# Performance work log

Hardware: AMD Instinct MI355X
Metric: run time of the kernel (lower is better)

The kernel has to match this reference:

```python
import jax, jax.numpy as jnp
import numpy as np

N_INP = 512
N_HID = 512
BATCH = 64
STEPS = 512


def setup_inputs() -> dict:
    key = jax.random.key(0)
    ks = jax.random.split(key, 7)

    def xavier(k, n_in, n_out):
        bound = np.sqrt(3.0) * np.sqrt(2.0 / float(n_in + n_out))
        return jax.random.uniform(k, (n_in, n_out), jnp.float32, -bound, bound)

    return {
        "inputs": jax.random.normal(ks[0], (BATCH, STEPS, N_INP), jnp.float32),
        "W_xz": xavier(ks[1], N_INP, N_HID),
        "W_hz": xavier(ks[2], N_HID, N_HID),
        "b_z": jnp.zeros((N_HID,), jnp.float32),
        "W_xr": xavier(ks[3], N_INP, N_HID),
        "W_hr": xavier(ks[4], N_HID, N_HID),
        "b_r": jnp.zeros((N_HID,), jnp.float32),
        "W_xh": xavier(ks[5], N_INP, N_HID),
        "W_hh": xavier(ks[6], N_HID, N_HID),
        "b_h": jnp.zeros((N_HID,), jnp.float32),
        "train": 0,
    }


def reference(inputs, W_xz, W_hz, b_z, W_xr, W_hr, b_r, W_xh, W_hh, b_h, train):
    # inputs: (B, T, n_inp). GRU with eval-mode (dropout_rate=0), so the
    # dropout branch in the original forward is a no-op.
    B = inputs.shape[0]
    H0 = jnp.zeros((B, W_hz.shape[0]), inputs.dtype)

    def step(H_t, X_t):
        Z_t = jax.nn.sigmoid(X_t @ W_xz + H_t @ W_hz + b_z)
        R_t = jax.nn.sigmoid(X_t @ W_xr + H_t @ W_hr + b_r)
        H_tilde = jnp.tanh(X_t @ W_xh + (R_t * H_t) @ W_hh + b_h)
        H_new = Z_t * H_t + (1.0 - Z_t) * H_tilde
        return H_new, H_new

    xs = jnp.swapaxes(inputs, 0, 1)  # (T, B, n_inp)
    H_final, outs = jax.lax.scan(step, H0, xs)
    outputs = jnp.swapaxes(outs, 0, 1)  # (B, T, n_hid)
    return outputs, H_final
```

## Files before the change

### kernel.cpp

```cpp
#include <hip/hip_runtime.h>

#define B_   64
#define T_   512
#define KIN  512
#define NH   512
#define KEFF 3072
#define NBLK 64
#define NTHR 512

typedef __attribute__((ext_vector_type(8))) short short8;
typedef __attribute__((ext_vector_type(4))) float f32x4;
typedef __attribute__((ext_vector_type(4))) unsigned int u32x4;

__device__ __forceinline__ unsigned short f2b(float f) {
    union { float f; unsigned int u; } v; v.f = f;
    unsigned int u = v.u;
    return (unsigned short)((u + 0x7FFFu + ((u >> 16) & 1u)) >> 16);
}
__device__ __forceinline__ float b2f(unsigned short h) {
    union { float f; unsigned int u; } v; v.u = ((unsigned int)h) << 16;
    return v.f;
}

__global__ void prepack(const float* __restrict__ Wxz, const float* __restrict__ Whz,
                        const float* __restrict__ Wxr, const float* __restrict__ Whr,
                        const float* __restrict__ Wxh, const float* __restrict__ Whh,
                        unsigned short* __restrict__ Bzr, unsigned short* __restrict__ Bh) {
    int keff = blockIdx.x * 256 + threadIdx.x;
    int n    = blockIdx.y;
    int seg  = keff >> 9;
    int k    = keff & 511;
    const float* src;
    int c;
    if (n < 512)       { c = n;        src = (seg < 3) ? Whz : Wxz; }
    else if (n < 1024) { c = n - 512;  src = (seg < 3) ? Whr : Wxr; }
    else               { c = n - 1024; src = (seg < 3) ? Whh : Wxh; }
    float w = src[k * NH + c];
    unsigned short hi = f2b(w);
    unsigned short o  = (seg == 2 || seg == 5) ? f2b(w - b2f(hi)) : hi;
    if (n < 1024) Bzr[(size_t)n * KEFF + keff] = o;
    else          Bh[(size_t)(n - 1024) * KEFF + keff] = o;
}

__device__ __forceinline__ unsigned int ald32(const unsigned int* p) {
    return __hip_atomic_load(p, __ATOMIC_RELAXED, __HIP_MEMORY_SCOPE_AGENT);
}
__device__ __forceinline__ unsigned long long ald64(const void* p) {
    return __hip_atomic_load((const unsigned long long*)p, __ATOMIC_RELAXED,
                             __HIP_MEMORY_SCOPE_AGENT);
}
__device__ __forceinline__ void ast32(unsigned int* p, unsigned int v) {
    __hip_atomic_store(p, v, __ATOMIC_RELAXED, __HIP_MEMORY_SCOPE_AGENT);
}
__device__ __forceinline__ void ast64(void* p, unsigned long long v) {
    __hip_atomic_store((unsigned long long*)p, v, __ATOMIC_RELAXED,
                       __HIP_MEMORY_SCOPE_AGENT);
}

__device__ __forceinline__ void flag_wait16(const unsigned int* flg,
                                            unsigned int tgt, int fidx) {
    while (1) {
        unsigned int v = ald32(flg + fidx);
        if (__all((int)(v >= tgt))) break;
    }
    __builtin_amdgcn_sched_barrier(0);
}

__device__ __forceinline__ int hp_idx(int m, int c) {
    return m * 512 + (c ^ ((m & 7) << 2));
}

__device__ __forceinline__ void cvt_x8(const float* xr, int kp, short8* ahi, short8* alo) {
    f32x4 x0 = *(const f32x4*)(xr + kp);
    f32x4 x1 = *(const f32x4*)(xr + kp + 4);
#pragma unroll
    for (int i = 0; i < 4; ++i) {
        unsigned short h0 = f2b(x0[i]);
        (*ahi)[i] = (short)h0; (*alo)[i] = (short)f2b(x0[i] - b2f(h0));
        unsigned short h1 = f2b(x1[i]);
        (*ahi)[4 + i] = (short)h1; (*alo)[4 + i] = (short)f2b(x1[i] - b2f(h1));
    }
}

__device__ __forceinline__ void unpackw(u32x4 w0, u32x4 w1, short8* ahi, short8* alo) {
    union { unsigned int u[4]; short8 v; } H, L;
    H.u[0] = __builtin_amdgcn_perm(w0[1], w0[0], 0x05040100u);
    H.u[1] = __builtin_amdgcn_perm(w0[3], w0[2], 0x05040100u);
    H.u[2] = __builtin_amdgcn_perm(w1[1], w1[0], 0x05040100u);
    H.u[3] = __builtin_amdgcn_perm(w1[3], w1[2], 0x05040100u);
    L.u[0] = __builtin_amdgcn_perm(w0[1], w0[0], 0x07060302u);
    L.u[1] = __builtin_amdgcn_perm(w0[3], w0[2], 0x07060302u);
    L.u[2] = __builtin_amdgcn_perm(w1[1], w1[0], 0x07060302u);
    L.u[3] = __builtin_amdgcn_perm(w1[3], w1[2], 0x07060302u);
    *ahi = H.v; *alo = L.v;
}

#define MFMA(a, b, c) __builtin_amdgcn_mfma_f32_16x16x32_bf16((a), (b), (c), 0, 0, 0)

__global__ void __launch_bounds__(NTHR, 2) gru_seq(
    const float* __restrict__ X, const float* __restrict__ bz,
    const float* __restrict__ br, const float* __restrict__ bh,
    float* __restrict__ out, float* __restrict__ Zt,
    unsigned int* __restrict__ HP, unsigned int* __restrict__ RHP,
    const unsigned short* __restrict__ Bzr, const unsigned short* __restrict__ Bh,
    unsigned int* flags) {
    const int bid  = blockIdx.x;
    const int s    = bid & 15;
    const int g    = bid >> 4;
    const int tid  = threadIdx.x;
    const int wv   = tid >> 6;
    const int w4   = wv & 3;
    const bool xc  = wv >= 4;
    const int lane = tid & 63;
    const int fm   = lane & 15;
    const int fkc  = lane >> 4;
    const int fk   = fkc * 8;

    __shared__ unsigned int hbufH[16 * 512];
    __shared__ unsigned int hbufR[16 * 512];
    __shared__ float xp1[2][4][16][16];
    __shared__ float xp2a[2][2][16][16];
    __shared__ float xp2b[2][2][16][16];
    __shared__ float comb[2][256];

    const int c1 = s * 64 + w4 * 16 + fm;
    const unsigned short* Bp1 = Bzr + (size_t)c1 * KEFF;
    const bool isz = (c1 < 512);
    const float bias1 = isz ? bz[c1] : br[c1 - 512];

    const int ti = w4 >> 1, jh = w4 & 1;
    const int c2 = s * 32 + ti * 16 + fm;
    const unsigned short* Bp2 = Bh + (size_t)c2 * KEFF;
    const float bias2 = bh[c2];

    const int key = (fm & 7) << 4;
    const int sw0 = (32 * fkc) ^ key;
    const int sw1 = (32 * fkc + 16) ^ key;

    unsigned int* HPg  = HP  + g * 8192;
    unsigned int* RHPg = RHP + g * 8192;
    float*        Ztg  = Zt  + g * 8192;
    unsigned int* flg  = flags + g * 32;
    const int fidx = (lane < 16) ? lane : 15;

    const float* Xg = X + (size_t)(16 * g + fm) * (T_ * KIN);

    auto xg1 = [&](int tt, int buf) {
        f32x4 acc = {0.f, 0.f, 0.f, 0.f};
        const float* xr = Xg + (size_t)tt * KIN;
#pragma unroll 4
        for (int j = 0; j < 16; ++j) {
            int kp = j * 32 + fk;
            short8 xhi, xlo; cvt_x8(xr, kp, &xhi, &xlo);
            short8 b3 = *(const short8*)(Bp1 + 1536 + kp);
            short8 b4 = *(const short8*)(Bp1 + 2048 + kp);
            short8 b5 = *(const short8*)(Bp1 + 2560 + kp);
            acc = MFMA(xhi, b3, acc); acc = MFMA(xlo, b4, acc); acc = MFMA(xhi, b5, acc);
        }
#pragma unroll
        for (int jj = 0; jj < 4; ++jj) xp1[buf][w4][fkc * 4 + jj][fm] = acc[jj];
    };
    auto xg2 = [&](int tt, int buf) {
        f32x4 acc = {0.f, 0.f, 0.f, 0.f};
        const float* xr = Xg + (size_t)tt * KIN;
#pragma unroll
        for (int j = jh * 8; j < jh * 8 + 8; ++j) {
            int kp = j * 32 + fk;
            short8 xhi, xlo; cvt_x8(xr, kp, &xhi, &xlo);
            short8 b3 = *(const short8*)(Bp2 + 1536 + kp);
            short8 b4 = *(const short8*)(Bp2 + 2048 + kp);
            short8 b5 = *(const short8*)(Bp2 + 2560 + kp);
            acc = MFMA(xhi, b3, acc); acc = MFMA(xlo, b4, acc); acc = MFMA(xhi, b5, acc);
        }
        float (*dst)[16][16] = jh ? xp2b[buf] : xp2a[buf];
#pragma unroll
        for (int jj = 0; jj < 4; ++jj) dst[ti][fkc * 4 + jj][fm] = acc[jj];
    };

    if (xc) { xg1(0, 0); xg2(0, 0); }
    __syncthreads();

    for (int t = 0; t < T_; ++t) {
        const int bufc = t & 1, bufn = bufc ^ 1;
        const unsigned int ep = (unsigned int)t * 2u;
        if (wv == 0 && t) flag_wait16(flg, ep, fidx);
        __syncthreads();
        if (!xc) {
            const char* srcb = (const char*)HPg;
            char* dstb = (char*)hbufH;
#pragma unroll
            for (int i = 0; i < 8; ++i) {
                int r = w4 * 8 + i;
                __builtin_amdgcn_global_load_lds(
                    (const unsigned int*)(srcb + r * 1024 + lane * 16),
                    (unsigned int*)(dstb + r * 1024), 16, 0, 0x11);
            }
            asm volatile("s_waitcnt vmcnt(0)" ::: "memory");
            __builtin_amdgcn_sched_barrier(0);
        }
        __syncthreads();
        if (!xc) {
            f32x4 acc = {0.f, 0.f, 0.f, 0.f};
            const char* sl = (const char*)hbufH + fm * 2048;
#pragma unroll 4
            for (int j = 0; j < 16; ++j) {
                u32x4 w0 = *(const u32x4*)(sl + 128 * j + sw0);
                u32x4 w1 = *(const u32x4*)(sl + 128 * j + sw1);
                short8 ahi, alo; unpackw(w0, w1, &ahi, &alo);
                int kp = j * 32 + fk;
                short8 b0 = *(const short8*)(Bp1 + kp);
                short8 b1 = *(const short8*)(Bp1 + 512 + kp);
                short8 b2 = *(const short8*)(Bp1 + 1024 + kp);
                acc = MFMA(ahi, b0, acc); acc = MFMA(alo, b1, acc); acc = MFMA(ahi, b2, acc);
            }
            if (isz) {
                float gz[4];
#pragma unroll
                for (int jj = 0; jj < 4; ++jj)
                    gz[jj] = 1.f / (1.f + __expf(-(acc[jj] +
                               xp1[bufc][w4][fkc * 4 + jj][fm] + bias1)));
                union { float f[2]; unsigned long long q; } p0, p1;
                p0.f[0] = gz[0]; p0.f[1] = gz[1];
                p1.f[0] = gz[2]; p1.f[1] = gz[3];
                float* zp = Ztg + c1 * 16 + fkc * 4;
                ast64(zp, p0.q); ast64(zp + 2, p1.q);
            } else {
                int cr = c1 - 512;
#pragma unroll
                for (int jj = 0; jj < 4; ++jj) {
                    int mr = fkc * 4 + jj;
                    unsigned int hw = *(const unsigned int*)((const char*)hbufH +
                        mr * 2048 + ((4 * cr) ^ ((mr & 7) << 4)));
                    float h  = b2f((unsigned short)(hw & 0xffffu)) +
                               b2f((unsigned short)(hw >> 16));
                    float gr = 1.f / (1.f + __expf(-(acc[jj] +
                                 xp1[bufc][w4][mr][fm] + bias1)));
                    float rh = gr * h;
                    unsigned short hi = f2b(rh);
                    unsigned short lo = f2b(rh - b2f(hi));
                    ast32(RHPg + hp_idx(mr, cr),
                          (unsigned int)hi | ((unsigned int)lo << 16));
                }
            }
        } else if (t + 1 < T_) {
            xg1(t + 1, bufn);
        }
        __syncthreads();
        if (tid == 0) ast32(flg + s, ep + 1u);
        if (wv == 0) flag_wait16(flg, ep + 1u, fidx);
        else if (xc && t + 1 < T_) xg2(t + 1, bufn);
        __syncthreads();
        unsigned long long zq0 = 0, zq1 = 0;
        if (!xc) {
            if (jh == 0) {
                const float* zp = Ztg + c2 * 16 + fkc * 4;
                zq0 = ald64(zp); zq1 = ald64(zp + 2);
            }
            const char* srcb = (const char*)RHPg;
            char* dstb = (char*)hbufR;
#pragma unroll
            for (int i = 0; i < 8; ++i) {
                int r = w4 * 8 + i;
                __builtin_amdgcn_global_load_lds(
                    (const unsigned int*)(srcb + r * 1024 + lane * 16),
                    (unsigned int*)(dstb + r * 1024), 16, 0, 0x11);
            }
            asm volatile("s_waitcnt vmcnt(0)" ::: "memory");
            __builtin_amdgcn_sched_barrier(0);
        }
        __syncthreads();
        f32x4 acc2 = {0.f, 0.f, 0.f, 0.f};
        if (!xc) {
            const char* sl2 = (const char*)hbufR + fm * 2048;
#pragma unroll
            for (int j = jh * 8; j < jh * 8 + 8; ++j) {
                u32x4 w0 = *(const u32x4*)(sl2 + 128 * j + sw0);
                u32x4 w1 = *(const u32x4*)(sl2 + 128 * j + sw1);
                short8 ahi, alo; unpackw(w0, w1, &ahi, &alo);
                int kp = j * 32 + fk;
                short8 b0 = *(const short8*)(Bp2 + kp);
                short8 b1 = *(const short8*)(Bp2 + 512 + kp);
                short8 b2 = *(const short8*)(Bp2 + 1024 + kp);
                acc2 = MFMA(ahi, b0, acc2); acc2 = MFMA(alo, b1, acc2); acc2 = MFMA(ahi, b2, acc2);
            }
            if (jh == 1) {
#pragma unroll
                for (int jj = 0; jj < 4; ++jj)
                    comb[ti][(fkc * 4 + jj) * 16 + fm] = acc2[jj];
            }
        }
        __syncthreads();
        if (!xc && jh == 0) {
            union { unsigned long long q; float f[2]; } z0, z1;
            z0.q = zq0; z1.q = zq1;
            float zv[4] = {z0.f[0], z0.f[1], z1.f[0], z1.f[1]};
#pragma unroll
            for (int jj = 0; jj < 4; ++jj) {
                int mr = fkc * 4 + jj;
                unsigned int hw = *(const unsigned int*)((const char*)hbufH +
                    mr * 2048 + ((4 * c2) ^ ((mr & 7) << 4)));
                float h   = b2f((unsigned short)(hw & 0xffffu)) +
                            b2f((unsigned short)(hw >> 16));
                float pre = acc2[jj] + comb[ti][mr * 16 + fm] +
                            xp2a[bufc][ti][mr][fm] + xp2b[bufc][ti][mr][fm] + bias2;
                float e   = __expf(-2.f * pre);
                float ht  = 2.f / (1.f + e) - 1.f;
                float hn  = zv[jj] * h + (1.f - zv[jj]) * ht;
                int mg = 16 * g + mr;
                out[(size_t)mg * (T_ * NH) + (size_t)t * NH + c2] = hn;
                if (t == T_ - 1)
                    out[(size_t)B_ * T_ * NH + mg * NH + c2] = hn;
                unsigned short hi = f2b(hn);
                unsigned short lo = f2b(hn - b2f(hi));
                ast32(HPg + hp_idx(mr, c2),
                      (unsigned int)hi | ((unsigned int)lo << 16));
            }
        }
        __syncthreads();
        if (tid == 0) ast32(flg + s, ep + 2u);
    }
}

extern "C" void kernel_launch(void* const* d_in, const int* in_sizes, int n_in,
                              void* d_out, int out_size, void* d_ws, size_t ws_size,
                              hipStream_t stream) {
    (void)in_sizes; (void)n_in; (void)out_size; (void)ws_size;
    const float* X   = (const float*)d_in[0];
    const float* Wxz = (const float*)d_in[1];
    const float* Whz = (const float*)d_in[2];
    const float* bz  = (const float*)d_in[3];
    const float* Wxr = (const float*)d_in[4];
    const float* Whr = (const float*)d_in[5];
    const float* br  = (const float*)d_in[6];
    const float* Wxh = (const float*)d_in[7];
    const float* Whh = (const float*)d_in[8];
    const float* bh  = (const float*)d_in[9];
    float* out = (float*)d_out;

    char* ws = (char*)d_ws;
    unsigned int* flags = (unsigned int*)ws;
    float* Zt         = (float*)(ws + 8192);
    unsigned int* HP  = (unsigned int*)(ws + 8192 + 131072);
    unsigned int* RHP = (unsigned int*)(ws + 8192 + 262144);
    unsigned short* Bzr = (unsigned short*)(ws + (1 << 20));
    unsigned short* Bh  = Bzr + (size_t)1024 * KEFF;

    hipMemsetAsync(d_ws, 0, 1 << 20, stream);
    prepack<<<dim3(12, 1536), 256, 0, stream>>>(Wxz, Whz, Wxr, Whr, Wxh, Whh, Bzr, Bh);
    gru_seq<<<NBLK, NTHR, 0, stream>>>(X, bz, br, bh, out, Zt, HP, RHP, Bzr, Bh, flags);
}
```

Baseline: 13.24 ms.

## Pipeline hidden-state staging in K-chunks and keep Z gate block-local

Each block now owns the z and r gate columns for its own 32 hidden units, so z stays in shared memory instead of going through a global Zt buffer. The hidden-state layout is reorganised into per-block slabs, and the LDS staging of H and R*H is split into four chunks that overlap with the MFMA work. Whole-group flag polling is replaced by per-chunk waits on the producer slabs that each chunk needs. The goal is to cut step latency on the serial recurrence, in exchange for more barriers per step and more complex flag ordering.

```diff
diff --git a/kernel.cpp b/kernel.cpp
--- a/kernel.cpp
+++ b/kernel.cpp
@@ -45,29 +45,22 @@
 __device__ __forceinline__ unsigned int ald32(const unsigned int* p) {
     return __hip_atomic_load(p, __ATOMIC_RELAXED, __HIP_MEMORY_SCOPE_AGENT);
 }
-__device__ __forceinline__ unsigned long long ald64(const void* p) {
-    return __hip_atomic_load((const unsigned long long*)p, __ATOMIC_RELAXED,
-                             __HIP_MEMORY_SCOPE_AGENT);
-}
 __device__ __forceinline__ void ast32(unsigned int* p, unsigned int v) {
     __hip_atomic_store(p, v, __ATOMIC_RELAXED, __HIP_MEMORY_SCOPE_AGENT);
 }
-__device__ __forceinline__ void ast64(void* p, unsigned long long v) {
-    __hip_atomic_store((unsigned long long*)p, v, __ATOMIC_RELAXED,
-                       __HIP_MEMORY_SCOPE_AGENT);
-}
-
-__device__ __forceinline__ void flag_wait16(const unsigned int* flg,
-                                            unsigned int tgt, int fidx) {
-    while (1) {
-        unsigned int v = ald32(flg + fidx);
-        if (__all((int)(v >= tgt))) break;
-    }
+
+__device__ __forceinline__ void barx() {
+    asm volatile("s_waitcnt lgkmcnt(0)" ::: "memory");
+    __builtin_amdgcn_s_barrier();
     __builtin_amdgcn_sched_barrier(0);
 }
-
-__device__ __forceinline__ int hp_idx(int m, int c) {
-    return m * 512 + (c ^ ((m & 7) << 2));
+__device__ __forceinline__ void vmdrain() {
+    asm volatile("s_waitcnt vmcnt(0)" ::: "memory");
+    __builtin_amdgcn_sched_barrier(0);
+}
+__device__ __forceinline__ void pollf(const unsigned int* p, unsigned int tgt) {
+    while (ald32(p) < tgt) { }
+    __builtin_amdgcn_sched_barrier(0);
 }
 
 __device__ __forceinline__ void cvt_x8(const float* xr, int kp, short8* ahi, short8* alo) {
@@ -100,7 +93,7 @@
 __global__ void __launch_bounds__(NTHR, 2) gru_seq(
     const float* __restrict__ X, const float* __restrict__ bz,
     const float* __restrict__ br, const float* __restrict__ bh,
-    float* __restrict__ out, float* __restrict__ Zt,
+    float* __restrict__ out,
     unsigned int* __restrict__ HP, unsigned int* __restrict__ RHP,
     const unsigned short* __restrict__ Bzr, const unsigned short* __restrict__ Bh,
     unsigned int* flags) {
@@ -121,202 +114,189 @@
     __shared__ float xp1[2][4][16][16];
     __shared__ float xp2a[2][2][16][16];
     __shared__ float xp2b[2][2][16][16];
+    __shared__ float zbufL[2][16][16];
     __shared__ float comb[2][256];
 
-    const int c1 = s * 64 + w4 * 16 + fm;
-    const unsigned short* Bp1 = Bzr + (size_t)c1 * KEFF;
-    const bool isz = (c1 < 512);
-    const float bias1 = isz ? bz[c1] : br[c1 - 512];
-
-    const int ti = w4 >> 1, jh = w4 & 1;
-    const int c2 = s * 32 + ti * 16 + fm;
+    const int half = w4 & 1;
+    const int gate = w4 >> 1;
+    const int c1l  = half * 16 + fm;
+    const unsigned short* Bp1 = Bzr + (size_t)(gate * 512 + s * 32 + c1l) * KEFF;
+    const float bias1 = gate ? br[s * 32 + c1l] : bz[s * 32 + c1l];
+
+    const int ti  = w4 >> 1, jh = w4 & 1;
+    const int c2l = ti * 16 + fm;
+    const int c2  = s * 32 + c2l;
     const unsigned short* Bp2 = Bh + (size_t)c2 * KEFF;
     const float bias2 = bh[c2];
 
-    const int key = (fm & 7) << 4;
-    const int sw0 = (32 * fkc) ^ key;
-    const int sw1 = (32 * fkc + 16) ^ key;
+    const int sw0 = (fkc * 32) ^ ((fm & 7) << 4);
+    const int sw1 = sw0 ^ 16;
 
     unsigned int* HPg  = HP  + g * 8192;
     unsigned int* RHPg = RHP + g * 8192;
-    float*        Ztg  = Zt  + g * 8192;
-    unsigned int* flg  = flags + g * 32;
-    const int fidx = (lane < 16) ? lane : 15;
+    unsigned int* flg  = flags + g * 64;
 
     const float* Xg = X + (size_t)(16 * g + fm) * (T_ * KIN);
 
-    auto xg1 = [&](int tt, int buf) {
-        f32x4 acc = {0.f, 0.f, 0.f, 0.f};
+    auto stage = [&](const unsigned int* gsrc, unsigned int* ldst, int grp) {
+        int slab = grp * 4 + w4;
+        const char* sp = (const char*)gsrc + slab * 2048 + lane * 16;
+        char* dp = (char*)ldst + slab * 2048;
+        __builtin_amdgcn_global_load_lds((const unsigned int*)sp,
+                                         (unsigned int*)dp, 16, 0, 0x11);
+        __builtin_amdgcn_global_load_lds((const unsigned int*)(sp + 1024),
+                                         (unsigned int*)(dp + 1024), 16, 0, 0x11);
+    };
+    auto gemmH = [&](const unsigned int* lbuf, const unsigned short* Bp,
+                     int slab, f32x4& a) {
+        const char* sb = (const char*)lbuf + slab * 2048 + fm * 128;
+        u32x4 w0 = *(const u32x4*)(sb + sw0);
+        u32x4 w1 = *(const u32x4*)(sb + sw1);
+        short8 ahi, alo; unpackw(w0, w1, &ahi, &alo);
+        const unsigned short* Bk = Bp + slab * 32 + fk;
+        short8 b0 = *(const short8*)(Bk);
+        short8 b1 = *(const short8*)(Bk + 512);
+        short8 b2 = *(const short8*)(Bk + 1024);
+        a = MFMA(ahi, b0, a); a = MFMA(alo, b1, a); a = MFMA(ahi, b2, a);
+    };
+    auto xg1p = [&](int gi, int tt, int buf, f32x4& a) {
         const float* xr = Xg + (size_t)tt * KIN;
-#pragma unroll 4
-        for (int j = 0; j < 16; ++j) {
-            int kp = j * 32 + fk;
+#pragma unroll
+        for (int q = 0; q < 4; ++q) {
+            int kp = (gi * 4 + q) * 32 + fk;
             short8 xhi, xlo; cvt_x8(xr, kp, &xhi, &xlo);
             short8 b3 = *(const short8*)(Bp1 + 1536 + kp);
             short8 b4 = *(const short8*)(Bp1 + 2048 + kp);
             short8 b5 = *(const short8*)(Bp1 + 2560 + kp);
-            acc = MFMA(xhi, b3, acc); acc = MFMA(xlo, b4, acc); acc = MFMA(xhi, b5, acc);
-        }
-#pragma unroll
-        for (int jj = 0; jj < 4; ++jj) xp1[buf][w4][fkc * 4 + jj][fm] = acc[jj];
+            a = MFMA(xhi, b3, a); a = MFMA(xlo, b4, a); a = MFMA(xhi, b5, a);
+        }
+        if (gi == 3) {
+#pragma unroll
+            for (int jj = 0; jj < 4; ++jj) xp1[buf][w4][fkc * 4 + jj][fm] = a[jj];
+        }
     };
-    auto xg2 = [&](int tt, int buf) {
-        f32x4 acc = {0.f, 0.f, 0.f, 0.f};
+    auto xg2p = [&](int gi, int tt, int buf, f32x4& a) {
         const float* xr = Xg + (size_t)tt * KIN;
 #pragma unroll
-        for (int j = jh * 8; j < jh * 8 + 8; ++j) {
-            int kp = j * 32 + fk;
+        for (int q = 0; q < 2; ++q) {
+            int kp = (jh * 8 + gi * 2 + q) * 32 + fk;
             short8 xhi, xlo; cvt_x8(xr, kp, &xhi, &xlo);
             short8 b3 = *(const short8*)(Bp2 + 1536 + kp);
             short8 b4 = *(const short8*)(Bp2 + 2048 + kp);
             short8 b5 = *(const short8*)(Bp2 + 2560 + kp);
-            acc = MFMA(xhi, b3, acc); acc = MFMA(xlo, b4, acc); acc = MFMA(xhi, b5, acc);
-        }
-        float (*dst)[16][16] = jh ? xp2b[buf] : xp2a[buf];
-#pragma unroll
-        for (int jj = 0; jj < 4; ++jj) dst[ti][fkc * 4 + jj][fm] = acc[jj];
+            a = MFMA(xhi, b3, a); a = MFMA(xlo, b4, a); a = MFMA(xhi, b5, a);
+        }
+        if (gi == 3) {
+            float (*dst)[16][16] = jh ? xp2b[buf] : xp2a[buf];
+#pragma unroll
+            for (int jj = 0; jj < 4; ++jj) dst[ti][fkc * 4 + jj][fm] = a[jj];
+        }
     };
 
-    if (xc) { xg1(0, 0); xg2(0, 0); }
-    __syncthreads();
+    if (xc) {
+        f32x4 a1 = {0.f, 0.f, 0.f, 0.f}, a2 = {0.f, 0.f, 0.f, 0.f};
+        for (int gi = 0; gi < 4; ++gi) { xg1p(gi, 0, 0, a1); xg2p(gi, 0, 0, a2); }
+    }
+    barx();
 
     for (int t = 0; t < T_; ++t) {
+        const unsigned int ep = (unsigned int)t * 2u;
         const int bufc = t & 1, bufn = bufc ^ 1;
-        const unsigned int ep = (unsigned int)t * 2u;
-        if (wv == 0 && t) flag_wait16(flg, ep, fidx);
-        __syncthreads();
+        const int tn = t + 1;
+        f32x4 acc = {0.f, 0.f, 0.f, 0.f}, ax1 = {0.f, 0.f, 0.f, 0.f};
+        if (xc) pollf(flg + w4, ep);
+        barx();
+        if (!xc) { stage(HPg, hbufH, 0); vmdrain(); }
+        else pollf(flg + 4 + w4, ep);
+        barx();
+        for (int gi = 0; gi < 4; ++gi) {
+            if (!xc) {
+                if (gi < 3) stage(HPg, hbufH, gi + 1);
+#pragma unroll
+                for (int q = 0; q < 4; ++q) gemmH(hbufH, Bp1, gi * 4 + q, acc);
+                if (gi < 3) vmdrain();
+            } else {
+                if (gi < 2) pollf(flg + 4 * (gi + 2) + w4, ep);
+                if (tn < T_) xg1p(gi, tn, bufn, ax1);
+            }
+            barx();
+        }
         if (!xc) {
-            const char* srcb = (const char*)HPg;
-            char* dstb = (char*)hbufH;
-#pragma unroll
-            for (int i = 0; i < 8; ++i) {
-                int r = w4 * 8 + i;
-                __builtin_amdgcn_global_load_lds(
-                    (const unsigned int*)(srcb + r * 1024 + lane * 16),
-                    (unsigned int*)(dstb + r * 1024), 16, 0, 0x11);
-            }
-            asm volatile("s_waitcnt vmcnt(0)" ::: "memory");
-            __builtin_amdgcn_sched_barrier(0);
-        }
-        __syncthreads();
-        if (!xc) {
-            f32x4 acc = {0.f, 0.f, 0.f, 0.f};
-            const char* sl = (const char*)hbufH + fm * 2048;
-#pragma unroll 4
-            for (int j = 0; j < 16; ++j) {
-                u32x4 w0 = *(const u32x4*)(sl + 128 * j + sw0);
-                u32x4 w1 = *(const u32x4*)(sl + 128 * j + sw1);
-                short8 ahi, alo; unpackw(w0, w1, &ahi, &alo);
-                int kp = j * 32 + fk;
-                short8 b0 = *(const short8*)(Bp1 + kp);
-                short8 b1 = *(const short8*)(Bp1 + 512 + kp);
-                short8 b2 = *(const short8*)(Bp1 + 1024 + kp);
-                acc = MFMA(ahi, b0, acc); acc = MFMA(alo, b1, acc); acc = MFMA(ahi, b2, acc);
-            }
-            if (isz) {
-                float gz[4];
-#pragma unroll
-                for (int jj = 0; jj < 4; ++jj)
-                    gz[jj] = 1.f / (1.f + __expf(-(acc[jj] +
-                               xp1[bufc][w4][fkc * 4 + jj][fm] + bias1)));
-                union { float f[2]; unsigned long long q; } p0, p1;
-                p0.f[0] = gz[0]; p0.f[1] = gz[1];
-                p1.f[0] = gz[2]; p1.f[1] = gz[3];
-                float* zp = Ztg + c1 * 16 + fkc * 4;
-                ast64(zp, p0.q); ast64(zp + 2, p1.q);
-            } else {
-                int cr = c1 - 512;
-#pragma unroll
-                for (int jj = 0; jj < 4; ++jj) {
-                    int mr = fkc * 4 + jj;
-                    unsigned int hw = *(const unsigned int*)((const char*)hbufH +
-                        mr * 2048 + ((4 * cr) ^ ((mr & 7) << 4)));
+#pragma unroll
+            for (int jj = 0; jj < 4; ++jj) {
+                int mr = fkc * 4 + jj;
+                float pre = acc[jj] + xp1[bufc][w4][mr][fm] + bias1;
+                float gv  = 1.f / (1.f + __expf(-pre));
+                if (gate == 0) {
+                    zbufL[half][mr][fm] = gv;
+                } else {
+                    unsigned int hw = hbufH[s * 512 + mr * 32 +
+                                            (c1l ^ ((mr & 7) << 2))];
                     float h  = b2f((unsigned short)(hw & 0xffffu)) +
                                b2f((unsigned short)(hw >> 16));
-                    float gr = 1.f / (1.f + __expf(-(acc[jj] +
-                                 xp1[bufc][w4][mr][fm] + bias1)));
-                    float rh = gr * h;
+                    float rh = gv * h;
                     unsigned short hi = f2b(rh);
                     unsigned short lo = f2b(rh - b2f(hi));
-                    ast32(RHPg + hp_idx(mr, cr),
+                    ast32(RHPg + s * 512 + mr * 32 + (c1l ^ ((mr & 7) << 2)),
                           (unsigned int)hi | ((unsigned int)lo << 16));
                 }
             }
-        } else if (t + 1 < T_) {
-            xg1(t + 1, bufn);
-        }
-        __syncthreads();
+            if (gate) vmdrain();
+        }
+        barx();
         if (tid == 0) ast32(flg + s, ep + 1u);
-        if (wv == 0) flag_wait16(flg, ep + 1u, fidx);
-        else if (xc && t + 1 < T_) xg2(t + 1, bufn);
-        __syncthreads();
-        unsigned long long zq0 = 0, zq1 = 0;
-        if (!xc) {
-            if (jh == 0) {
-                const float* zp = Ztg + c2 * 16 + fkc * 4;
-                zq0 = ald64(zp); zq1 = ald64(zp + 2);
+        f32x4 acc2 = {0.f, 0.f, 0.f, 0.f}, ax2 = {0.f, 0.f, 0.f, 0.f};
+        if (xc) pollf(flg + w4, ep + 1u);
+        barx();
+        if (!xc) { stage(RHPg, hbufR, 0); vmdrain(); }
+        else pollf(flg + 4 + w4, ep + 1u);
+        barx();
+        for (int gi = 0; gi < 4; ++gi) {
+            if (!xc) {
+                if (gi < 3) stage(RHPg, hbufR, gi + 1);
+                if ((gi >> 1) == jh) {
+#pragma unroll
+                    for (int q = 0; q < 4; ++q) gemmH(hbufR, Bp2, gi * 4 + q, acc2);
+                }
+                if (gi < 3) vmdrain();
+            } else {
+                if (gi < 2) pollf(flg + 4 * (gi + 2) + w4, ep + 1u);
+                if (tn < T_) xg2p(gi, tn, bufn, ax2);
             }
-            const char* srcb = (const char*)RHPg;
-            char* dstb = (char*)hbufR;
-#pragma unroll
-            for (int i = 0; i < 8; ++i) {
-                int r = w4 * 8 + i;
-                __builtin_amdgcn_global_load_lds(
-                    (const unsigned int*)(srcb + r * 1024 + lane * 16),
-                    (unsigned int*)(dstb + r * 1024), 16, 0, 0x11);
-            }
-            asm volatile("s_waitcnt vmcnt(0)" ::: "memory");
-            __builtin_amdgcn_sched_barrier(0);
-        }
-        __syncthreads();
-        f32x4 acc2 = {0.f, 0.f, 0.f, 0.f};
-        if (!xc) {
-            const char* sl2 = (const char*)hbufR + fm * 2048;
-#pragma unroll
-            for (int j = jh * 8; j < jh * 8 + 8; ++j) {
-                u32x4 w0 = *(const u32x4*)(sl2 + 128 * j + sw0);
-                u32x4 w1 = *(const u32x4*)(sl2 + 128 * j + sw1);
-                short8 ahi, alo; unpackw(w0, w1, &ahi, &alo);
-                int kp = j * 32 + fk;
-                short8 b0 = *(const short8*)(Bp2 + kp);
-                short8 b1 = *(const short8*)(Bp2 + 512 + kp);
-                short8 b2 = *(const short8*)(Bp2 + 1024 + kp);
-                acc2 = MFMA(ahi, b0, acc2); acc2 = MFMA(alo, b1, acc2); acc2 = MFMA(ahi, b2, acc2);
-            }
-            if (jh == 1) {
-#pragma unroll
-                for (int jj = 0; jj < 4; ++jj)
-                    comb[ti][(fkc * 4 + jj) * 16 + fm] = acc2[jj];
-            }
-        }
-        __syncthreads();
+            barx();
+        }
+        if (!xc && jh == 1) {
+#pragma unroll
+            for (int jj = 0; jj < 4; ++jj)
+                comb[ti][(fkc * 4 + jj) * 16 + fm] = acc2[jj];
+        }
+        barx();
         if (!xc && jh == 0) {
-            union { unsigned long long q; float f[2]; } z0, z1;
-            z0.q = zq0; z1.q = zq1;
-            float zv[4] = {z0.f[0], z0.f[1], z1.f[0], z1.f[1]};
 #pragma unroll
             for (int jj = 0; jj < 4; ++jj) {
                 int mr = fkc * 4 + jj;
-                unsigned int hw = *(const unsigned int*)((const char*)hbufH +
-                    mr * 2048 + ((4 * c2) ^ ((mr & 7) << 4)));
+                unsigned int hw = hbufH[s * 512 + mr * 32 +
+                                        (c2l ^ ((mr & 7) << 2))];
                 float h   = b2f((unsigned short)(hw & 0xffffu)) +
                             b2f((unsigned short)(hw >> 16));
                 float pre = acc2[jj] + comb[ti][mr * 16 + fm] +
                             xp2a[bufc][ti][mr][fm] + xp2b[bufc][ti][mr][fm] + bias2;
                 float e   = __expf(-2.f * pre);
                 float ht  = 2.f / (1.f + e) - 1.f;
-                float hn  = zv[jj] * h + (1.f - zv[jj]) * ht;
+                float z   = zbufL[ti][mr][fm];
+                float hn  = z * h + (1.f - z) * ht;
                 int mg = 16 * g + mr;
                 out[(size_t)mg * (T_ * NH) + (size_t)t * NH + c2] = hn;
                 if (t == T_ - 1)
                     out[(size_t)B_ * T_ * NH + mg * NH + c2] = hn;
                 unsigned short hi = f2b(hn);
                 unsigned short lo = f2b(hn - b2f(hi));
-                ast32(HPg + hp_idx(mr, c2),
+                ast32(HPg + s * 512 + mr * 32 + (c2l ^ ((mr & 7) << 2)),
                       (unsigned int)hi | ((unsigned int)lo << 16));
             }
-        }
-        __syncthreads();
+            vmdrain();
+        }
+        barx();
         if (tid == 0) ast32(flg + s, ep + 2u);
     }
 }
@@ -339,13 +319,12 @@
 
     char* ws = (char*)d_ws;
     unsigned int* flags = (unsigned int*)ws;
-    float* Zt         = (float*)(ws + 8192);
-    unsigned int* HP  = (unsigned int*)(ws + 8192 + 131072);
-    unsigned int* RHP = (unsigned int*)(ws + 8192 + 262144);
+    unsigned int* HP  = (unsigned int*)(ws + 4096);
+    unsigned int* RHP = (unsigned int*)(ws + 4096 + 131072);
     unsigned short* Bzr = (unsigned short*)(ws + (1 << 20));
     unsigned short* Bh  = Bzr + (size_t)1024 * KEFF;
 
     hipMemsetAsync(d_ws, 0, 1 << 20, stream);
     prepack<<<dim3(12, 1536), 256, 0, stream>>>(Wxz, Whz, Wxr, Whr, Wxh, Whh, Bzr, Bh);
-    gru_seq<<<NBLK, NTHR, 0, stream>>>(X, bz, br, bh, out, Zt, HP, RHP, Bzr, Bh, flags);
-}
+    gru_seq<<<NBLK, NTHR, 0, stream>>>(X, bz, br, bh, out, HP, RHP, Bzr, Bh, flags);
+}
```

New measurement: 15.66 ms. +18.3%, slower.
